# Optimization experiments

Measured on AMD Instinct MI355X. Metric: run time of the kernel, lower is better.

## Reference

```python
import jax, jax.numpy as jnp
import numpy as np

B, C, IMG, P = 8, 6, 384, 16
DIM, HEADS, DEPTH, MLP, NCLS = 768, 12, 4, 3072, 1000
N = (IMG // P) ** 2            # 576 patches
DH = DIM // HEADS              # 64
PATCH_DIM = C * P * P          # 1536


def setup_inputs() -> dict:
    key = jax.random.key(0)
    ks = jax.random.split(key, 13)
    f = lambda k, shp, s=0.02: jax.random.normal(k, shp, jnp.float32) * s
    return {
        "x": jax.random.normal(ks[0], (B, C, IMG, IMG), jnp.float32),
        "patch_w": f(ks[1], (PATCH_DIM, DIM)),
        "patch_b": f(ks[2], (DIM,)),
        "ln1_g": jnp.ones((DEPTH, DIM), jnp.float32),
        "ln1_b": jnp.zeros((DEPTH, DIM), jnp.float32),
        "w_qkv": f(ks[3], (DEPTH, DIM, 3 * DIM)),
        "bias_att": f(ks[4], (DEPTH, HEADS, N, N), 0.5),
        "w_out": f(ks[5], (DEPTH, DIM, DIM)),
        "ln2_g": jnp.ones((DEPTH, DIM), jnp.float32),
        "ln2_b": jnp.zeros((DEPTH, DIM), jnp.float32),
        "w1": f(ks[6], (DEPTH, DIM, MLP)),
        "b1": f(ks[7], (DEPTH, MLP)),
        "w2": f(ks[8], (DEPTH, MLP, DIM)),
        "b2": f(ks[9], (DEPTH, DIM)),
        "lnh_g": jnp.ones((DIM,), jnp.float32),
        "lnh_b": jnp.zeros((DIM,), jnp.float32),
        "w_head": f(ks[10], (DIM, NCLS)),
        "b_head": f(ks[11], (NCLS,)),
    }


def _ln(x, g, b, eps=1e-5):
    m = x.mean(-1, keepdims=True)
    v = ((x - m) ** 2).mean(-1, keepdims=True)
    return (x - m) * jax.lax.rsqrt(v + eps) * g + b


def _patchify(x, patch_w, patch_b):
    # Rearrange 'b c (h p1) (w p2) -> b (h w) (p1 p2 c)' then Linear(patch_dim, dim)
    b = x.shape[0]
    g = IMG // P
    x = x.reshape(b, C, g, P, g, P).transpose(0, 2, 4, 3, 5, 1).reshape(b, g * g, PATCH_DIM)
    return x @ patch_w + patch_b


def _forward(x, patch_w, patch_b, ln1_g, ln1_b, w_qkv, bias_att, w_out,
             ln2_g, ln2_b, w1, b1, w2, b2, lnh_g, lnh_b, w_head, b_head):
    scale = DH ** -0.5
    tok = _patchify(x, patch_w, patch_b)  # [B, N, DIM]; pos_info='mul_att_normed' -> no pos_embed added

    def block(t, p):
        l1g, l1b, wqkv, bias, wout, l2g, l2b, ww1, bb1, ww2, bb2 = p
        h = _ln(t, l1g, l1b)
        qkv = h @ wqkv                                     # [B, N, 3*DIM]
        q, k, v = jnp.split(qkv, 3, axis=-1)
        rs = lambda a: a.reshape(t.shape[0], N, HEADS, DH).transpose(0, 2, 1, 3)
        q, k, v = rs(q), rs(k), rs(v)                      # [B, H, N, DH]
        dots = jnp.einsum('bhid,bhjd->bhij', q, k) * scale
        # mul_att_normed: softmax(qk) * softmax(bias), renormalized over keys
        attn = jax.nn.softmax(dots, axis=-1) * jax.nn.softmax(bias, axis=-1)[None]
        attn = attn / attn.sum(-1, keepdims=True)
        o = jnp.einsum('bhij,bhjd->bhid', attn, v)
        o = o.transpose(0, 2, 1, 3).reshape(t.shape[0], N, DIM) @ wout
        t = t + o
        h2 = _ln(t, l2g, l2b)
        t = t + (jax.nn.gelu(h2 @ ww1 + bb1, approximate=False) @ ww2 + bb2)
        return t, None

    tok, _ = jax.lax.scan(block, tok,
                          (ln1_g, ln1_b, w_qkv, bias_att, w_out,
                           ln2_g, ln2_b, w1, b1, w2, b2))
    pooled = tok.mean(axis=1)                              # mean-pool tokens
    return _ln(pooled, lnh_g, lnh_b) @ w_head + b_head     # [B, NCLS]


def reference(x, patch_w, patch_b, ln1_g, ln1_b, w_qkv, bias_att, w_out,
              ln2_g, ln2_b, w1, b1, w2, b2, lnh_g, lnh_b, w_head, b_head):
    return _forward(x, patch_w, patch_b, ln1_g, ln1_b, w_qkv, bias_att, w_out,
                    ln2_g, ln2_b, w1, b1, w2, b2, lnh_g, lnh_b, w_head, b_head)
```

## Files before the change

kernel.cpp:

```cpp
#include <hip/hip_runtime.h>
#include <hip/hip_bf16.h>

typedef __attribute__((ext_vector_type(8))) short bf16x8;
typedef __attribute__((ext_vector_type(4))) float f32x4;

#define DEVI __device__ __forceinline__

DEVI unsigned short f2bf_bits(float f) {
    __hip_bfloat16 h = __float2bfloat16(f);
    return *reinterpret_cast<unsigned short*>(&h);
}

DEVI void gload_lds16(const void* g, void* lds) {
    __builtin_amdgcn_global_load_lds(
        (const __attribute__((address_space(1))) unsigned int*)g,
        (__attribute__((address_space(3))) unsigned int*)lds, 16, 0, 0);
}

template <int N> DEVI void wait_vm() {
    if constexpr (N == 0) asm volatile("s_waitcnt vmcnt(0)" ::: "memory");
    else if constexpr (N == 3) asm volatile("s_waitcnt vmcnt(3)" ::: "memory");
    else if constexpr (N == 4) asm volatile("s_waitcnt vmcnt(4)" ::: "memory");
    else if constexpr (N == 6) asm volatile("s_waitcnt vmcnt(6)" ::: "memory");
    else if constexpr (N == 8) asm volatile("s_waitcnt vmcnt(8)" ::: "memory");
    __builtin_amdgcn_sched_barrier(0);
}

__global__ __launch_bounds__(256) void patchify_kernel(const float* __restrict__ x,
                                                       unsigned short* __restrict__ patches)
{
    size_t i = (size_t)blockIdx.x * 256 + threadIdx.x;
    int j = (int)(i % 384);
    size_t t = i / 384;
    int r = (int)(t % 384); t /= 384;
    int c = (int)(t % 6);
    int b = (int)(t / 6);
    int gh = r >> 4, p1 = r & 15, gw = j >> 4, p2 = j & 15;
    int prow = b * 576 + gh * 24 + gw;
    int pcol = (p1 * 16 + p2) * 6 + c;
    patches[(size_t)prow * 1536 + pcol] = f2bf_bits(x[i]);
}

DEVI void convT_body(const float* __restrict__ W, __hip_bfloat16* __restrict__ Wt,
                     int K, int N, int k0, int n0, int tid)
{
    __shared__ float tile[32][33];
    int tx = tid & 31, ty = tid >> 5;
#pragma unroll
    for (int i = 0; i < 4; i++)
        tile[ty + 8 * i][tx] = W[(size_t)(k0 + ty + 8 * i) * N + n0 + tx];
    __syncthreads();
#pragma unroll
    for (int i = 0; i < 4; i++)
        Wt[(size_t)(n0 + ty + 8 * i) * K + k0 + tx] = __float2bfloat16(tile[tx][ty + 8 * i]);
}

__global__ __launch_bounds__(256) void convT_kernel(const float* __restrict__ W,
                                                    __hip_bfloat16* __restrict__ Wt,
                                                    int K, int N)
{
    convT_body(W, Wt, K, N, blockIdx.y * 32, blockIdx.x * 32, threadIdx.x);
}

__global__ __launch_bounds__(256) void convT4_kernel(const float* __restrict__ wqkv,
                                                     const float* __restrict__ wout,
                                                     const float* __restrict__ w1,
                                                     const float* __restrict__ w2,
                                                     __hip_bfloat16* __restrict__ dst)
{
    int bt = blockIdx.x;
    const float* W; __hip_bfloat16* Wt; int K, N, lt;
    if (bt < 1728)      { W = wqkv; K = 768;  N = 2304; lt = bt;        Wt = dst; }
    else if (bt < 2304) { W = wout; K = 768;  N = 768;  lt = bt - 1728; Wt = dst + 1769472; }
    else if (bt < 4608) { W = w1;   K = 768;  N = 3072; lt = bt - 2304; Wt = dst + 2359296; }
    else                { W = w2;   K = 3072; N = 768;  lt = bt - 4608; Wt = dst + 4718592; }
    int tn = N >> 5;
    convT_body(W, Wt, K, N, (lt / tn) * 32, (lt % tn) * 32, threadIdx.x);
}

DEVI void st_ln(float* p, float v) { *p = v; }
DEVI void st_ln(__hip_bfloat16* p, float v) { *p = __float2bfloat16(v); }

template <typename OutT>
__global__ __launch_bounds__(256) void ln_kernel(const float* __restrict__ x,
                                                 const float* __restrict__ g,
                                                 const float* __restrict__ b,
                                                 OutT* __restrict__ out)
{
    int row = blockIdx.x, tid = threadIdx.x;
    const float* xr = x + (size_t)row * 768;
    float v0 = xr[tid], v1 = xr[tid + 256], v2 = xr[tid + 512];
    float s = v0 + v1 + v2;
    float s2 = v0 * v0 + v1 * v1 + v2 * v2;
#pragma unroll
    for (int m = 32; m >= 1; m >>= 1) { s += __shfl_xor(s, m); s2 += __shfl_xor(s2, m); }
    __shared__ float red[8];
    int w = tid >> 6;
    if ((tid & 63) == 0) { red[w] = s; red[4 + w] = s2; }
    __syncthreads();
    s = red[0] + red[1] + red[2] + red[3];
    s2 = red[4] + red[5] + red[6] + red[7];
    float mean = s * (1.0f / 768.0f);
    float var = s2 * (1.0f / 768.0f) - mean * mean;
    float rstd = rsqrtf(var + 1e-5f);
    OutT* orow = out + (size_t)row * 768;
    st_ln(&orow[tid], (v0 - mean) * rstd * g[tid] + b[tid]);
    st_ln(&orow[tid + 256], (v1 - mean) * rstd * g[tid + 256] + b[tid + 256]);
    st_ln(&orow[tid + 512], (v2 - mean) * rstd * g[tid + 512] + b[tid + 512]);
}

template <int BM, bool BIAS, bool RESID, bool GELU, bool BF16OUT>
__global__ __launch_bounds__(256, 3) void gemm_bt_kernel(
    const __hip_bfloat16* __restrict__ A,
    const __hip_bfloat16* __restrict__ Bt,
    const float* __restrict__ bias,
    const float* __restrict__ resid,
    float* __restrict__ Cf,
    __hip_bfloat16* __restrict__ Cb,
    int M, int N, int K, int gx, int chunk)
{
    constexpr int MREP = BM / 32;
    constexpr int SL = BM / 64 + 2;
    __shared__ __align__(16) __hip_bfloat16 As[3][BM * 32];
    __shared__ __align__(16) __hip_bfloat16 Bs[3][128 * 32];
    const int tid = threadIdx.x;
    const int wid = tid >> 6, lane = tid & 63;
    const int g = lane >> 4, l16 = lane & 15;
    const int wm = (wid >> 1) * (BM / 2), wn = (wid & 1) * 64;

    const int seq = (blockIdx.x & 7) * chunk + (blockIdx.x >> 3);
    const int bm = (seq / gx) * BM, bn = (seq % gx) * 128;

    const int sr = tid >> 2;
    const int csrc = (lane & 3) ^ ((lane >> 3) & 3);
    const int sdst = sr * 32 + (lane & 3) * 8;
    size_t aOff[BM / 64], bOff[2];
#pragma unroll
    for (int i = 0; i < BM / 64; i++) aOff[i] = (size_t)(bm + i * 64 + sr) * K + csrc * 8;
#pragma unroll
    for (int i = 0; i < 2; i++)       bOff[i] = (size_t)(bn + i * 64 + sr) * K + csrc * 8;

    auto stage = [&](__hip_bfloat16* asb, __hip_bfloat16* bsb, int tq) {
        const __hip_bfloat16* ap = A + tq * 32;
        const __hip_bfloat16* bp = Bt + tq * 32;
#pragma unroll
        for (int i = 0; i < BM / 64; i++) gload_lds16(ap + aOff[i], asb + i * 2048 + sdst);
#pragma unroll
        for (int i = 0; i < 2; i++)       gload_lds16(bp + bOff[i], bsb + i * 2048 + sdst);
    };

    const int pSw = (l16 >> 1) & 3;
    f32x4 acc[MREP][4] = {};
    const int nt = K >> 5;

    stage(As[0], Bs[0], 0);
    stage(As[1], Bs[1], 1);
    stage(As[2], Bs[2], 2);
    wait_vm<2 * SL>();
    __builtin_amdgcn_s_barrier();
    __builtin_amdgcn_sched_barrier(0);

    for (int t = 0; t < nt; t += 3) {
#pragma unroll
        for (int u = 0; u < 3; u++) {
            const int tc = t + u;
            bf16x8 af[MREP], bfr[4];
#pragma unroll
            for (int mi = 0; mi < MREP; mi++)
                af[mi] = *(const bf16x8*)&As[u][(wm + mi * 16 + l16) * 32 + ((g ^ pSw) << 3)];
#pragma unroll
            for (int ni = 0; ni < 4; ni++)
                bfr[ni] = *(const bf16x8*)&Bs[u][(wn + ni * 16 + l16) * 32 + ((g ^ pSw) << 3)];
#pragma unroll
            for (int mi = 0; mi < MREP; mi++)
#pragma unroll
                for (int ni = 0; ni < 4; ni++)
                    acc[mi][ni] = __builtin_amdgcn_mfma_f32_16x16x32_bf16(af[mi], bfr[ni], acc[mi][ni], 0, 0, 0);

            asm volatile("s_waitcnt lgkmcnt(0)" ::: "memory");
            __builtin_amdgcn_sched_barrier(0);
            __builtin_amdgcn_s_barrier();
            __builtin_amdgcn_sched_barrier(0);

            if (tc + 3 < nt) stage(As[u], Bs[u], tc + 3);
            if (tc + 1 < nt) {
                if (tc + 4 <= nt)      wait_vm<2 * SL>();
                else if (tc + 3 == nt) wait_vm<SL>();
                else                   wait_vm<0>();
                __builtin_amdgcn_s_barrier();
                __builtin_amdgcn_sched_barrier(0);
            }
        }
    }

#pragma unroll
    for (int mi = 0; mi < MREP; mi++) {
#pragma unroll
        for (int ni = 0; ni < 4; ni++) {
            int gcol = bn + wn + ni * 16 + l16;
            float bval = 0.0f;
            if (BIAS) bval = bias[gcol];
#pragma unroll
            for (int r = 0; r < 4; r++) {
                int grow = bm + wm + mi * 16 + 4 * g + r;
                float v = acc[mi][ni][r] + bval;
                if (GELU) v = 0.5f * v * (1.0f + erff(v * 0.70710678118654752f));
                if (RESID) v += resid[(size_t)grow * N + gcol];
                if (BF16OUT) Cb[(size_t)grow * N + gcol] = __float2bfloat16(v);
                else Cf[(size_t)grow * N + gcol] = v;
            }
        }
    }
}

__global__ __launch_bounds__(256) void attn_kernel(const __hip_bfloat16* __restrict__ qkvb,
                                                   const float* __restrict__ bias,
                                                   unsigned short* __restrict__ o)
{
    const int seq = (blockIdx.x & 7) * 108 + (blockIdx.x >> 3);
    const int bb = seq & 7, qt = (seq >> 3) % 9, h = seq / 72;
    const int q0 = qt * 64;
    const int tid = threadIdx.x;
    const int wq = tid >> 6, lane = tid & 63, g = lane >> 4, l16 = lane & 15;

    __shared__ __align__(16) unsigned short Qs[64 * 72];
    __shared__ __align__(16) unsigned short Ks[64 * 72];
    __shared__ __align__(16) unsigned short Vt[64 * 72];
    __shared__ __align__(16) unsigned short Ps[4][16 * 72];

    {
        int r = tid >> 2, cb = (tid & 3) * 16;
        const int4* s4 = (const int4*)&qkvb[(size_t)(bb * 576 + q0 + r) * 2304 + h * 64 + cb];
        int4* d4 = (int4*)&Qs[r * 72 + cb];
        d4[0] = s4[0]; d4[1] = s4[1];
    }
    __syncthreads();
    bf16x8 qf0 = *(const bf16x8*)&Qs[(wq * 16 + l16) * 72 + g * 8];
    bf16x8 qf1 = *(const bf16x8*)&Qs[(wq * 16 + l16) * 72 + 32 + g * 8];

    float m_r[4] = {-1e30f, -1e30f, -1e30f, -1e30f};
    float l_r[4] = {0.f, 0.f, 0.f, 0.f};
    f32x4 oa[4] = {};
    const float* bias_h = bias + (size_t)h * 576 * 576;
    const float scale = 0.125f;

    for (int kt = 0; kt < 576; kt += 64) {
        {
            int r = tid >> 2, cb = (tid & 3) * 16;
            const int4* s4 = (const int4*)&qkvb[(size_t)(bb * 576 + kt + r) * 2304 + 768 + h * 64 + cb];
            int4* d4 = (int4*)&Ks[r * 72 + cb];
            d4[0] = s4[0]; d4[1] = s4[1];
            int key = tid & 63, d0 = (tid >> 6) * 16;
            const unsigned short* vs = (const unsigned short*)&qkvb[(size_t)(bb * 576 + kt + key) * 2304 + 1536 + h * 64 + d0];
            bf16x8 v0 = *(const bf16x8*)vs;
            bf16x8 v1 = *(const bf16x8*)(vs + 8);
#pragma unroll
            for (int e = 0; e < 8; e++) {
                Vt[(d0 + e) * 72 + key] = (unsigned short)v0[e];
                Vt[(d0 + 8 + e) * 72 + key] = (unsigned short)v1[e];
            }
        }
        __syncthreads();

        float bl[4][4];
#pragma unroll
        for (int kc = 0; kc < 4; kc++)
#pragma unroll
            for (int r = 0; r < 4; r++) {
                int q = q0 + wq * 16 + 4 * g + r;
                bl[kc][r] = bias_h[(size_t)q * 576 + kt + kc * 16 + l16];
            }

        f32x4 sc[4] = {};
#pragma unroll
        for (int kc = 0; kc < 4; kc++) {
            bf16x8 kf0 = *(const bf16x8*)&Ks[(kc * 16 + l16) * 72 + g * 8];
            bf16x8 kf1 = *(const bf16x8*)&Ks[(kc * 16 + l16) * 72 + 32 + g * 8];
            sc[kc] = __builtin_amdgcn_mfma_f32_16x16x32_bf16(qf0, kf0, sc[kc], 0, 0, 0);
            sc[kc] = __builtin_amdgcn_mfma_f32_16x16x32_bf16(qf1, kf1, sc[kc], 0, 0, 0);
        }

        float sv[4][4], mt[4] = {-1e30f, -1e30f, -1e30f, -1e30f};
#pragma unroll
        for (int kc = 0; kc < 4; kc++)
#pragma unroll
            for (int r = 0; r < 4; r++) {
                float s = sc[kc][r] * scale + bl[kc][r];
                sv[kc][r] = s;
                mt[r] = fmaxf(mt[r], s);
            }
#pragma unroll
        for (int r = 0; r < 4; r++)
#pragma unroll
            for (int m = 1; m < 16; m <<= 1) mt[r] = fmaxf(mt[r], __shfl_xor(mt[r], m));

        float sf[4];
#pragma unroll
        for (int r = 0; r < 4; r++) {
            float mn = fmaxf(m_r[r], mt[r]);
            sf[r] = __expf(m_r[r] - mn);
            m_r[r] = mn;
        }
        float rs[4] = {0.f, 0.f, 0.f, 0.f};
#pragma unroll
        for (int kc = 0; kc < 4; kc++)
#pragma unroll
            for (int r = 0; r < 4; r++) {
                float p = __expf(sv[kc][r] - m_r[r]);
                rs[r] += p;
                Ps[wq][(4 * g + r) * 72 + kc * 16 + l16] = f2bf_bits(p);
            }
#pragma unroll
        for (int r = 0; r < 4; r++) {
#pragma unroll
            for (int m = 1; m < 16; m <<= 1) rs[r] += __shfl_xor(rs[r], m);
            l_r[r] = l_r[r] * sf[r] + rs[r];
        }
#pragma unroll
        for (int dt = 0; dt < 4; dt++)
#pragma unroll
            for (int r = 0; r < 4; r++) oa[dt][r] *= sf[r];

        asm volatile("s_waitcnt lgkmcnt(0)" ::: "memory");

#pragma unroll
        for (int s = 0; s < 2; s++) {
            bf16x8 pf = *(const bf16x8*)&Ps[wq][l16 * 72 + s * 32 + g * 8];
#pragma unroll
            for (int dt = 0; dt < 4; dt++) {
                bf16x8 vf = *(const bf16x8*)&Vt[(dt * 16 + l16) * 72 + s * 32 + g * 8];
                oa[dt] = __builtin_amdgcn_mfma_f32_16x16x32_bf16(pf, vf, oa[dt], 0, 0, 0);
            }
        }
        __syncthreads();
    }

#pragma unroll
    for (int dt = 0; dt < 4; dt++)
#pragma unroll
        for (int r = 0; r < 4; r++) {
            int q = q0 + wq * 16 + 4 * g + r;
            float v = oa[dt][r] / l_r[r];
            o[(size_t)(bb * 576 + q) * 768 + h * 64 + dt * 16 + l16] = f2bf_bits(v);
        }
}

__global__ __launch_bounds__(256) void pool_kernel(const float* __restrict__ tok, float* __restrict__ pooled)
{
    int d = blockIdx.x * 256 + threadIdx.x;
    int b = blockIdx.y;
    float s = 0.0f;
    for (int n = 0; n < 576; n++) s += tok[(size_t)(b * 576 + n) * 768 + d];
    pooled[b * 768 + d] = s * (1.0f / 576.0f);
}

__global__ __launch_bounds__(256) void head_kernel(const float* __restrict__ lnp,
                                                   const float* __restrict__ w,
                                                   const float* __restrict__ bh,
                                                   float* __restrict__ out)
{
    int c = blockIdx.x * 256 + threadIdx.x;
    int b = blockIdx.y;
    if (c >= 1000) return;
    float s = bh[c];
    for (int d = 0; d < 768; d++) s += lnp[b * 768 + d] * w[(size_t)d * 1000 + c];
    out[b * 1000 + c] = s;
}

extern "C" void kernel_launch(void* const* d_in, const int* in_sizes, int n_in,
                              void* d_out, int out_size, void* d_ws, size_t ws_size,
                              hipStream_t stream)
{
    const float* x = (const float*)d_in[0];
    const float* patch_w = (const float*)d_in[1];
    const float* patch_b = (const float*)d_in[2];
    const float* ln1_g = (const float*)d_in[3];
    const float* ln1_b = (const float*)d_in[4];
    const float* w_qkv = (const float*)d_in[5];
    const float* bias_att = (const float*)d_in[6];
    const float* w_out = (const float*)d_in[7];
    const float* ln2_g = (const float*)d_in[8];
    const float* ln2_b = (const float*)d_in[9];
    const float* w1 = (const float*)d_in[10];
    const float* b1 = (const float*)d_in[11];
    const float* w2 = (const float*)d_in[12];
    const float* b2 = (const float*)d_in[13];
    const float* lnh_g = (const float*)d_in[14];
    const float* lnh_b = (const float*)d_in[15];
    const float* w_head = (const float*)d_in[16];
    const float* b_head = (const float*)d_in[17];
    float* out = (float*)d_out;

    char* ws = (char*)d_ws;
    float* tok = (float*)(ws + 0);
    __hip_bfloat16* qkv_bf = (__hip_bfloat16*)(ws + 14155776);
    float* pooled = (float*)(ws + 56623104);
    float* pooledln = (float*)(ws + 56647680);
    __hip_bfloat16* patches = (__hip_bfloat16*)(ws + 56672256);
    __hip_bfloat16* lw = patches;
    __hip_bfloat16* h_bf = (__hip_bfloat16*)(ws + 70828032);
    __hip_bfloat16* o_bf = (__hip_bfloat16*)(ws + 77905920);
    __hip_bfloat16* hid_bf = (__hip_bfloat16*)(ws + 84983808);
    __hip_bfloat16* wbuf = (__hip_bfloat16*)(ws + 113295360);

    patchify_kernel<<<27648, 256, 0, stream>>>(x, (unsigned short*)patches);
    convT_kernel<<<dim3(768 / 32, 1536 / 32), 256, 0, stream>>>(patch_w, wbuf, 1536, 768);
    gemm_bt_kernel<64, true, false, false, false><<<432, 256, 0, stream>>>(
        patches, wbuf, patch_b, nullptr, tok, nullptr, 4608, 768, 1536, 6, 54);

    for (int l = 0; l < 4; l++) {
        convT4_kernel<<<6912, 256, 0, stream>>>(
            w_qkv + (size_t)l * 768 * 2304, w_out + (size_t)l * 768 * 768,
            w1 + (size_t)l * 768 * 3072, w2 + (size_t)l * 3072 * 768, lw);
        ln_kernel<__hip_bfloat16><<<4608, 256, 0, stream>>>(tok, ln1_g + l * 768, ln1_b + l * 768, h_bf);
        gemm_bt_kernel<128, false, false, false, true><<<648, 256, 0, stream>>>(
            h_bf, lw, nullptr, nullptr, nullptr, qkv_bf, 4608, 2304, 768, 18, 81);
        attn_kernel<<<864, 256, 0, stream>>>(
            qkv_bf, bias_att + (size_t)l * 12 * 576 * 576, (unsigned short*)o_bf);
        gemm_bt_kernel<64, false, true, false, false><<<432, 256, 0, stream>>>(
            o_bf, lw + 1769472, nullptr, tok, tok, nullptr, 4608, 768, 768, 6, 54);
        ln_kernel<__hip_bfloat16><<<4608, 256, 0, stream>>>(tok, ln2_g + l * 768, ln2_b + l * 768, h_bf);
        gemm_bt_kernel<128, true, false, true, true><<<864, 256, 0, stream>>>(
            h_bf, lw + 2359296, b1 + l * 3072, nullptr, nullptr, hid_bf, 4608, 3072, 768, 24, 108);
        gemm_bt_kernel<64, true, true, false, false><<<432, 256, 0, stream>>>(
            hid_bf, lw + 4718592, b2 + l * 768, tok, tok, nullptr, 4608, 768, 3072, 6, 54);
    }

    pool_kernel<<<dim3(3, 8), 256, 0, stream>>>(tok, pooled);
    ln_kernel<float><<<8, 256, 0, stream>>>(pooled, lnh_g, lnh_b, pooledln);
    head_kernel<<<dim3(4, 8), 256, 0, stream>>>(pooledln, w_head, b_head, out);
}
```

Before: 921.2 us.

## Add 128x256 wide GEMM, grouped tile remap, vectorized patchify, MFMA priority hints

Replaces the 128-row GEMM used for the QKV and MLP-up projections with a 128x256 tile kernel that writes bf16 output through LDS as coalesced 16-byte stores. Replaces the chunked block ordering with a grouped 2D remap so neighbouring blocks share A rows. Patchify now reads 8 floats and writes 8 contiguous bf16 values per thread, using a c-major column order, and the patch weight transpose permutes its rows to match. It also raises wave priority around MFMA sections in the GEMM and attention kernels. The larger tile needs more registers and LDS per block (occupancy hint drops to 2) and launches fewer blocks, which may leave CUs underused.

```diff
diff --git a/kernel.cpp b/kernel.cpp
--- a/kernel.cpp
+++ b/kernel.cpp
@@ -20,25 +20,56 @@
 template <int N> DEVI void wait_vm() {
     if constexpr (N == 0) asm volatile("s_waitcnt vmcnt(0)" ::: "memory");
     else if constexpr (N == 3) asm volatile("s_waitcnt vmcnt(3)" ::: "memory");
-    else if constexpr (N == 4) asm volatile("s_waitcnt vmcnt(4)" ::: "memory");
     else if constexpr (N == 6) asm volatile("s_waitcnt vmcnt(6)" ::: "memory");
-    else if constexpr (N == 8) asm volatile("s_waitcnt vmcnt(8)" ::: "memory");
+    else if constexpr (N == 12) asm volatile("s_waitcnt vmcnt(12)" ::: "memory");
     __builtin_amdgcn_sched_barrier(0);
+}
+
+DEVI int2 remap2d(int bid, int total, int gx) {
+    int q = total >> 3, r = total & 7, x = bid & 7, l = bid >> 3;
+    int seq = (x < r ? x * (q + 1) : r * (q + 1) + (x - r) * q) + l;
+    int g4 = seq / (4 * gx);
+    int rem = seq - g4 * 4 * gx;
+    return {g4 * 4 + (rem & 3), rem >> 2};
 }
 
 __global__ __launch_bounds__(256) void patchify_kernel(const float* __restrict__ x,
                                                        unsigned short* __restrict__ patches)
 {
-    size_t i = (size_t)blockIdx.x * 256 + threadIdx.x;
-    int j = (int)(i % 384);
-    size_t t = i / 384;
+    size_t t8 = (size_t)blockIdx.x * 256 + threadIdx.x;
+    int jq = (int)(t8 % 48);
+    size_t t = t8 / 48;
     int r = (int)(t % 384); t /= 384;
     int c = (int)(t % 6);
     int b = (int)(t / 6);
+    int j = jq * 8;
     int gh = r >> 4, p1 = r & 15, gw = j >> 4, p2 = j & 15;
     int prow = b * 576 + gh * 24 + gw;
-    int pcol = (p1 * 16 + p2) * 6 + c;
-    patches[(size_t)prow * 1536 + pcol] = f2bf_bits(x[i]);
+    int pcol = c * 256 + p1 * 16 + p2;
+    const float* src = x + ((((size_t)b * 6 + c) * 384 + r) * 384 + j);
+    float4 v0 = ((const float4*)src)[0];
+    float4 v1 = ((const float4*)src)[1];
+    ushort u[8] = { f2bf_bits(v0.x), f2bf_bits(v0.y), f2bf_bits(v0.z), f2bf_bits(v0.w),
+                    f2bf_bits(v1.x), f2bf_bits(v1.y), f2bf_bits(v1.z), f2bf_bits(v1.w) };
+    *(int4*)&patches[(size_t)prow * 1536 + pcol] = *(int4*)u;
+}
+
+__global__ __launch_bounds__(256) void convT_patch_kernel(const float* __restrict__ W,
+                                                          __hip_bfloat16* __restrict__ Wt)
+{
+    __shared__ float tile[32][33];
+    int n0 = blockIdx.x * 32, kp0 = blockIdx.y * 32;
+    int tx = threadIdx.x & 31, ty = threadIdx.x >> 5;
+#pragma unroll
+    for (int i = 0; i < 4; i++) {
+        int kp = kp0 + ty + 8 * i;
+        int k = (kp & 255) * 6 + (kp >> 8);
+        tile[ty + 8 * i][tx] = W[(size_t)k * 768 + n0 + tx];
+    }
+    __syncthreads();
+#pragma unroll
+    for (int i = 0; i < 4; i++)
+        Wt[(size_t)(n0 + ty + 8 * i) * 1536 + kp0 + tx] = __float2bfloat16(tile[tx][ty + 8 * i]);
 }
 
 DEVI void convT_body(const float* __restrict__ W, __hip_bfloat16* __restrict__ Wt,
@@ -53,13 +84,6 @@
 #pragma unroll
     for (int i = 0; i < 4; i++)
         Wt[(size_t)(n0 + ty + 8 * i) * K + k0 + tx] = __float2bfloat16(tile[tx][ty + 8 * i]);
-}
-
-__global__ __launch_bounds__(256) void convT_kernel(const float* __restrict__ W,
-                                                    __hip_bfloat16* __restrict__ Wt,
-                                                    int K, int N)
-{
-    convT_body(W, Wt, K, N, blockIdx.y * 32, blockIdx.x * 32, threadIdx.x);
 }
 
 __global__ __launch_bounds__(256) void convT4_kernel(const float* __restrict__ wqkv,
@@ -109,48 +133,44 @@
     st_ln(&orow[tid + 512], (v2 - mean) * rstd * g[tid + 512] + b[tid + 512]);
 }
 
-template <int BM, bool BIAS, bool RESID, bool GELU, bool BF16OUT>
+template <bool BIAS, bool RESID, bool GELU>
 __global__ __launch_bounds__(256, 3) void gemm_bt_kernel(
     const __hip_bfloat16* __restrict__ A,
     const __hip_bfloat16* __restrict__ Bt,
     const float* __restrict__ bias,
     const float* __restrict__ resid,
     float* __restrict__ Cf,
-    __hip_bfloat16* __restrict__ Cb,
-    int M, int N, int K, int gx, int chunk)
-{
-    constexpr int MREP = BM / 32;
-    constexpr int SL = BM / 64 + 2;
+    int M, int N, int K, int gx)
+{
+    constexpr int BM = 64, SL = 3;
     __shared__ __align__(16) __hip_bfloat16 As[3][BM * 32];
     __shared__ __align__(16) __hip_bfloat16 Bs[3][128 * 32];
     const int tid = threadIdx.x;
     const int wid = tid >> 6, lane = tid & 63;
     const int g = lane >> 4, l16 = lane & 15;
-    const int wm = (wid >> 1) * (BM / 2), wn = (wid & 1) * 64;
-
-    const int seq = (blockIdx.x & 7) * chunk + (blockIdx.x >> 3);
-    const int bm = (seq / gx) * BM, bn = (seq % gx) * 128;
+    const int wm = (wid >> 1) * 32, wn = (wid & 1) * 64;
+
+    int2 bc = remap2d(blockIdx.x, gridDim.x, gx);
+    const int bm = bc.x * BM, bn = bc.y * 128;
 
     const int sr = tid >> 2;
     const int csrc = (lane & 3) ^ ((lane >> 3) & 3);
     const int sdst = sr * 32 + (lane & 3) * 8;
-    size_t aOff[BM / 64], bOff[2];
-#pragma unroll
-    for (int i = 0; i < BM / 64; i++) aOff[i] = (size_t)(bm + i * 64 + sr) * K + csrc * 8;
-#pragma unroll
-    for (int i = 0; i < 2; i++)       bOff[i] = (size_t)(bn + i * 64 + sr) * K + csrc * 8;
+    size_t aOff = (size_t)(bm + sr) * K + csrc * 8;
+    size_t bOff[2];
+#pragma unroll
+    for (int i = 0; i < 2; i++) bOff[i] = (size_t)(bn + i * 64 + sr) * K + csrc * 8;
 
     auto stage = [&](__hip_bfloat16* asb, __hip_bfloat16* bsb, int tq) {
         const __hip_bfloat16* ap = A + tq * 32;
         const __hip_bfloat16* bp = Bt + tq * 32;
-#pragma unroll
-        for (int i = 0; i < BM / 64; i++) gload_lds16(ap + aOff[i], asb + i * 2048 + sdst);
-#pragma unroll
-        for (int i = 0; i < 2; i++)       gload_lds16(bp + bOff[i], bsb + i * 2048 + sdst);
+        gload_lds16(ap + aOff, asb + sdst);
+#pragma unroll
+        for (int i = 0; i < 2; i++) gload_lds16(bp + bOff[i], bsb + i * 2048 + sdst);
     };
 
     const int pSw = (l16 >> 1) & 3;
-    f32x4 acc[MREP][4] = {};
+    f32x4 acc[2][4] = {};
     const int nt = K >> 5;
 
     stage(As[0], Bs[0], 0);
@@ -164,18 +184,20 @@
 #pragma unroll
         for (int u = 0; u < 3; u++) {
             const int tc = t + u;
-            bf16x8 af[MREP], bfr[4];
-#pragma unroll
-            for (int mi = 0; mi < MREP; mi++)
+            bf16x8 af[2], bfr[4];
+#pragma unroll
+            for (int mi = 0; mi < 2; mi++)
                 af[mi] = *(const bf16x8*)&As[u][(wm + mi * 16 + l16) * 32 + ((g ^ pSw) << 3)];
 #pragma unroll
             for (int ni = 0; ni < 4; ni++)
                 bfr[ni] = *(const bf16x8*)&Bs[u][(wn + ni * 16 + l16) * 32 + ((g ^ pSw) << 3)];
-#pragma unroll
-            for (int mi = 0; mi < MREP; mi++)
+            __builtin_amdgcn_s_setprio(1);
+#pragma unroll
+            for (int mi = 0; mi < 2; mi++)
 #pragma unroll
                 for (int ni = 0; ni < 4; ni++)
                     acc[mi][ni] = __builtin_amdgcn_mfma_f32_16x16x32_bf16(af[mi], bfr[ni], acc[mi][ni], 0, 0, 0);
+            __builtin_amdgcn_s_setprio(0);
 
             asm volatile("s_waitcnt lgkmcnt(0)" ::: "memory");
             __builtin_amdgcn_sched_barrier(0);
@@ -194,7 +216,7 @@
     }
 
 #pragma unroll
-    for (int mi = 0; mi < MREP; mi++) {
+    for (int mi = 0; mi < 2; mi++) {
 #pragma unroll
         for (int ni = 0; ni < 4; ni++) {
             int gcol = bn + wn + ni * 16 + l16;
@@ -206,10 +228,122 @@
                 float v = acc[mi][ni][r] + bval;
                 if (GELU) v = 0.5f * v * (1.0f + erff(v * 0.70710678118654752f));
                 if (RESID) v += resid[(size_t)grow * N + gcol];
-                if (BF16OUT) Cb[(size_t)grow * N + gcol] = __float2bfloat16(v);
-                else Cf[(size_t)grow * N + gcol] = v;
-            }
-        }
+                Cf[(size_t)grow * N + gcol] = v;
+            }
+        }
+    }
+}
+
+template <bool BIAS, bool GELU>
+__global__ __launch_bounds__(256, 2) void gemm_wide_kernel(
+    const __hip_bfloat16* __restrict__ A,
+    const __hip_bfloat16* __restrict__ Bt,
+    const float* __restrict__ bias,
+    __hip_bfloat16* __restrict__ Cb,
+    int M, int N, int K, int gx)
+{
+    constexpr int SL = 6;
+    __shared__ __align__(16) __hip_bfloat16 As[3][128 * 32];
+    __shared__ __align__(16) __hip_bfloat16 Bs[3][256 * 32];
+    const int tid = threadIdx.x;
+    const int wid = tid >> 6, lane = tid & 63;
+    const int g = lane >> 4, l16 = lane & 15;
+    const int wm = (wid >> 1) * 64, wn = (wid & 1) * 128;
+
+    int2 bc = remap2d(blockIdx.x, gridDim.x, gx);
+    const int bm = bc.x * 128, bn = bc.y * 256;
+
+    const int sr = tid >> 2;
+    const int csrc = (lane & 3) ^ ((lane >> 3) & 3);
+    const int sdst = sr * 32 + (lane & 3) * 8;
+    size_t aOff[2], bOff[4];
+#pragma unroll
+    for (int i = 0; i < 2; i++) aOff[i] = (size_t)(bm + i * 64 + sr) * K + csrc * 8;
+#pragma unroll
+    for (int i = 0; i < 4; i++) bOff[i] = (size_t)(bn + i * 64 + sr) * K + csrc * 8;
+
+    auto stage = [&](__hip_bfloat16* asb, __hip_bfloat16* bsb, int tq) {
+        const __hip_bfloat16* ap = A + tq * 32;
+        const __hip_bfloat16* bp = Bt + tq * 32;
+#pragma unroll
+        for (int i = 0; i < 2; i++) gload_lds16(ap + aOff[i], asb + i * 2048 + sdst);
+#pragma unroll
+        for (int i = 0; i < 4; i++) gload_lds16(bp + bOff[i], bsb + i * 2048 + sdst);
+    };
+
+    const int pSw = (l16 >> 1) & 3;
+    f32x4 acc[4][8] = {};
+    const int nt = K >> 5;
+
+    stage(As[0], Bs[0], 0);
+    stage(As[1], Bs[1], 1);
+    stage(As[2], Bs[2], 2);
+    wait_vm<2 * SL>();
+    __builtin_amdgcn_s_barrier();
+    __builtin_amdgcn_sched_barrier(0);
+
+    for (int t = 0; t < nt; t += 3) {
+#pragma unroll
+        for (int u = 0; u < 3; u++) {
+            const int tc = t + u;
+            bf16x8 af[4], bfr[8];
+#pragma unroll
+            for (int mi = 0; mi < 4; mi++)
+                af[mi] = *(const bf16x8*)&As[u][(wm + mi * 16 + l16) * 32 + ((g ^ pSw) << 3)];
+#pragma unroll
+            for (int ni = 0; ni < 8; ni++)
+                bfr[ni] = *(const bf16x8*)&Bs[u][(wn + ni * 16 + l16) * 32 + ((g ^ pSw) << 3)];
+            __builtin_amdgcn_s_setprio(1);
+#pragma unroll
+            for (int mi = 0; mi < 4; mi++)
+#pragma unroll
+                for (int ni = 0; ni < 8; ni++)
+                    acc[mi][ni] = __builtin_amdgcn_mfma_f32_16x16x32_bf16(af[mi], bfr[ni], acc[mi][ni], 0, 0, 0);
+            __builtin_amdgcn_s_setprio(0);
+
+            asm volatile("s_waitcnt lgkmcnt(0)" ::: "memory");
+            __builtin_amdgcn_sched_barrier(0);
+            __builtin_amdgcn_s_barrier();
+            __builtin_amdgcn_sched_barrier(0);
+
+            if (tc + 3 < nt) stage(As[u], Bs[u], tc + 3);
+            if (tc + 1 < nt) {
+                if (tc + 4 <= nt)      wait_vm<2 * SL>();
+                else if (tc + 3 == nt) wait_vm<SL>();
+                else                   wait_vm<0>();
+                __builtin_amdgcn_s_barrier();
+                __builtin_amdgcn_sched_barrier(0);
+            }
+        }
+    }
+
+    __hip_bfloat16* scr = &As[0][0] + wid * (16 * 136);
+#pragma unroll
+    for (int mi = 0; mi < 4; mi++) {
+#pragma unroll
+        for (int ni = 0; ni < 8; ni++) {
+            int gcol = bn + wn + ni * 16 + l16;
+            float bval = 0.0f;
+            if (BIAS) bval = bias[gcol];
+#pragma unroll
+            for (int r = 0; r < 4; r++) {
+                float v = acc[mi][ni][r] + bval;
+                if (GELU) v = 0.5f * v * (1.0f + erff(v * 0.70710678118654752f));
+                scr[(4 * g + r) * 136 + ni * 16 + l16] = __float2bfloat16(v);
+            }
+        }
+        asm volatile("s_waitcnt lgkmcnt(0)" ::: "memory");
+        __builtin_amdgcn_sched_barrier(0);
+#pragma unroll
+        for (int q2 = 0; q2 < 4; q2++) {
+            int idx = q2 * 64 + lane;
+            int row16 = idx >> 4, ch = idx & 15;
+            bf16x8 vv = *(const bf16x8*)&scr[row16 * 136 + ch * 8];
+            int grow = bm + wm + mi * 16 + row16;
+            *(int4*)&Cb[(size_t)grow * N + bn + wn + ch * 8] = *(int4*)&vv;
+        }
+        asm volatile("s_waitcnt lgkmcnt(0)" ::: "memory");
+        __builtin_amdgcn_sched_barrier(0);
     }
 }
 
@@ -272,6 +406,7 @@
             }
 
         f32x4 sc[4] = {};
+        __builtin_amdgcn_s_setprio(1);
 #pragma unroll
         for (int kc = 0; kc < 4; kc++) {
             bf16x8 kf0 = *(const bf16x8*)&Ks[(kc * 16 + l16) * 72 + g * 8];
@@ -279,6 +414,7 @@
             sc[kc] = __builtin_amdgcn_mfma_f32_16x16x32_bf16(qf0, kf0, sc[kc], 0, 0, 0);
             sc[kc] = __builtin_amdgcn_mfma_f32_16x16x32_bf16(qf1, kf1, sc[kc], 0, 0, 0);
         }
+        __builtin_amdgcn_s_setprio(0);
 
         float sv[4][4], mt[4] = {-1e30f, -1e30f, -1e30f, -1e30f};
 #pragma unroll
@@ -323,6 +459,7 @@
 
         asm volatile("s_waitcnt lgkmcnt(0)" ::: "memory");
 
+        __builtin_amdgcn_s_setprio(1);
 #pragma unroll
         for (int s = 0; s < 2; s++) {
             bf16x8 pf = *(const bf16x8*)&Ps[wq][l16 * 72 + s * 32 + g * 8];
@@ -332,6 +469,7 @@
                 oa[dt] = __builtin_amdgcn_mfma_f32_16x16x32_bf16(pf, vf, oa[dt], 0, 0, 0);
             }
         }
+        __builtin_amdgcn_s_setprio(0);
         __syncthreads();
     }
 
@@ -403,27 +541,27 @@
     __hip_bfloat16* hid_bf = (__hip_bfloat16*)(ws + 84983808);
     __hip_bfloat16* wbuf = (__hip_bfloat16*)(ws + 113295360);
 
-    patchify_kernel<<<27648, 256, 0, stream>>>(x, (unsigned short*)patches);
-    convT_kernel<<<dim3(768 / 32, 1536 / 32), 256, 0, stream>>>(patch_w, wbuf, 1536, 768);
-    gemm_bt_kernel<64, true, false, false, false><<<432, 256, 0, stream>>>(
-        patches, wbuf, patch_b, nullptr, tok, nullptr, 4608, 768, 1536, 6, 54);
+    patchify_kernel<<<3456, 256, 0, stream>>>(x, (unsigned short*)patches);
+    convT_patch_kernel<<<dim3(24, 48), 256, 0, stream>>>(patch_w, wbuf);
+    gemm_bt_kernel<true, false, false><<<432, 256, 0, stream>>>(
+        patches, wbuf, patch_b, nullptr, tok, 4608, 768, 1536, 6);
 
     for (int l = 0; l < 4; l++) {
         convT4_kernel<<<6912, 256, 0, stream>>>(
             w_qkv + (size_t)l * 768 * 2304, w_out + (size_t)l * 768 * 768,
             w1 + (size_t)l * 768 * 3072, w2 + (size_t)l * 3072 * 768, lw);
         ln_kernel<__hip_bfloat16><<<4608, 256, 0, stream>>>(tok, ln1_g + l * 768, ln1_b + l * 768, h_bf);
-        gemm_bt_kernel<128, false, false, false, true><<<648, 256, 0, stream>>>(
-            h_bf, lw, nullptr, nullptr, nullptr, qkv_bf, 4608, 2304, 768, 18, 81);
+        gemm_wide_kernel<false, false><<<324, 256, 0, stream>>>(
+            h_bf, lw, nullptr, qkv_bf, 4608, 2304, 768, 9);
         attn_kernel<<<864, 256, 0, stream>>>(
             qkv_bf, bias_att + (size_t)l * 12 * 576 * 576, (unsigned short*)o_bf);
-        gemm_bt_kernel<64, false, true, false, false><<<432, 256, 0, stream>>>(
-            o_bf, lw + 1769472, nullptr, tok, tok, nullptr, 4608, 768, 768, 6, 54);
+        gemm_bt_kernel<false, true, false><<<432, 256, 0, stream>>>(
+            o_bf, lw + 1769472, nullptr, tok, tok, 4608, 768, 768, 6);
         ln_kernel<__hip_bfloat16><<<4608, 256, 0, stream>>>(tok, ln2_g + l * 768, ln2_b + l * 768, h_bf);
-        gemm_bt_kernel<128, true, false, true, true><<<864, 256, 0, stream>>>(
-            h_bf, lw + 2359296, b1 + l * 3072, nullptr, nullptr, hid_bf, 4608, 3072, 768, 24, 108);
-        gemm_bt_kernel<64, true, true, false, false><<<432, 256, 0, stream>>>(
-            hid_bf, lw + 4718592, b2 + l * 768, tok, tok, nullptr, 4608, 768, 3072, 6, 54);
+        gemm_wide_kernel<true, true><<<432, 256, 0, stream>>>(
+            h_bf, lw + 2359296, b1 + l * 3072, hid_bf, 4608, 3072, 768, 12);
+        gemm_bt_kernel<true, true, false><<<432, 256, 0, stream>>>(
+            hid_bf, lw + 4718592, b2 + l * 768, tok, tok, 4608, 768, 3072, 6);
     }
 
     pool_kernel<<<dim3(3, 8), 256, 0, stream>>>(tok, pooled);
```

After: 910.3 us. Within noise of the previous version (-1.2%).
